# Kernel optimization log

Hardware: AMD Instinct MI355X
Metric: run time of the kernel (lower is better)

The kernel has to match this reference:

```python
import jax, jax.numpy as jnp
import numpy as np

DIM_BODY = 10
DIM_OBJECT = 15
NB_OBJECTS = 3
FIRST_INDS = np.array([0,1,2,3,4,5,6,7,8,9,10,11,12,13,15,16,17,20,21,25])
SECOND_INDS = np.array([0,1,2,3,4,5,6,7,8,9,14,18,19,22,23,24,26,27,28,29])
LOG_SIG_MIN, LOG_SIG_MAX = -20.0, 2.0


def setup_inputs() -> dict:
    key = jax.random.key(0)
    ks = jax.random.split(key, 16)
    B = 65536
    s = 0.05  # weight scale, keeps activations sane
    return {
        "obs": jax.random.normal(ks[0], (B, DIM_BODY + NB_OBJECTS * DIM_OBJECT), jnp.float32),
        "ag": jax.random.normal(ks[1], (B, 30), jnp.float32),
        "g": jax.random.normal(ks[2], (B, 30), jnp.float32),
        "phi_w1": jax.random.normal(ks[3], (80, 256), jnp.float32) * s,
        "phi_b1": jnp.zeros((256,), jnp.float32),
        "phi_w2": jax.random.normal(ks[4], (256, 256), jnp.float32) * s,
        "phi_b2": jnp.zeros((256,), jnp.float32),
        "rho_w1": jax.random.normal(ks[5], (256, 256), jnp.float32) * s,
        "rho_b1": jnp.zeros((256,), jnp.float32),
        "mean_w": jax.random.normal(ks[6], (256, 4), jnp.float32) * s,
        "mean_b": jnp.zeros((4,), jnp.float32),
        "logstd_w": jax.random.normal(ks[7], (256, 4), jnp.float32) * s,
        "logstd_b": jnp.zeros((4,), jnp.float32),
    }


def reference(obs, ag, g, phi_w1, phi_b1, phi_w2, phi_b2, rho_w1, rho_b1,
              mean_w, mean_b, logstd_w, logstd_b):
    body = obs[:, :DIM_BODY]  # [B,10]
    objs = [obs[:, DIM_BODY + DIM_OBJECT * i: DIM_BODY + DIM_OBJECT * (i + 1)]
            for i in range(NB_OBJECTS)]
    ag_f, g_f = ag[:, FIRST_INDS], g[:, FIRST_INDS]
    ag_s, g_s = ag[:, SECOND_INDS], g[:, SECOND_INDS]
    pair_inputs = []
    for i in range(NB_OBJECTS):
        for j in range(NB_OBJECTS):
            if i < j:
                pair_inputs.append(jnp.concatenate([ag_f, body, g_f, objs[i], objs[j]], axis=1))
            elif j < i:
                pair_inputs.append(jnp.concatenate([ag_s, body, g_s, objs[i], objs[j]], axis=1))
    inp = jnp.stack(pair_inputs)  # [6, B, 80]
    # shared phi MLP (2 layers, ReLU on both)
    h = jax.nn.relu(jnp.einsum('pbi,ih->pbh', inp, phi_w1) + phi_b1)
    phi = jax.nn.relu(jnp.einsum('pbh,ho->pbo', h, phi_w2) + phi_b2)
    agg = phi.sum(axis=0)  # [B, 256] sum over pairs
    # rho head
    hr = jax.nn.relu(agg @ rho_w1 + rho_b1)
    mean = hr @ mean_w + mean_b
    logstd = jnp.clip(hr @ logstd_w + logstd_b, LOG_SIG_MIN, LOG_SIG_MAX)
    return mean, logstd
```

## Files before the change

### kernel.cpp

```cpp
#include <hip/hip_runtime.h>
#include <hip/hip_bf16.h>


#define B_TOTAL 65536
#define TROWS   64

typedef __attribute__((ext_vector_type(8)))  short s8v;
typedef __attribute__((ext_vector_type(16))) float f16v;

__constant__ int c_PI[6] = {0,0,1,1,2,2};
__constant__ int c_PJ[6] = {1,2,0,2,0,1};
__constant__ int c_PF[6] = {0,0,1,0,1,1};
__constant__ int c_INV[2][30] = {
  {0,1,2,3,4,5,6,7,8,9,10,11,12,13,-1,14,15,16,-1,-1,17,18,-1,-1,-1,19,-1,-1,-1,-1},
  {0,1,2,3,4,5,6,7,8,9,-1,-1,-1,-1,10,-1,-1,-1,11,12,-1,-1,13,14,15,-1,16,17,18,19}};

static __device__ __forceinline__ short bf16s(float v) {
  __hip_bfloat16 h = __float2bfloat16(v);
  union { __hip_bfloat16 h; short s; } u; u.h = h; return u.s;
}
static __device__ __forceinline__ unsigned pk2(float a, float b) {
  __hip_bfloat162 h = __float22bfloat162_rn(float2{a, b});
  union { __hip_bfloat162 h2; unsigned u; } cv; cv.h2 = h;
  return cv.u;
}

__global__ __launch_bounds__(256)
void prep_weights(const float* __restrict__ phi_w1,
                  const float* __restrict__ phi_b1,
                  const float* __restrict__ phi_w2,
                  const float* __restrict__ rho_w1,
                  const float* __restrict__ mean_w,
                  const float* __restrict__ logstd_w,
                  __hip_bfloat16* __restrict__ W1P,
                  __hip_bfloat16* __restrict__ W2f,
                  __hip_bfloat16* __restrict__ W3f,
                  __hip_bfloat16* __restrict__ W4f) {
  const int wid  = (blockIdx.x * blockDim.x + threadIdx.x) >> 6;
  const int lane = threadIdx.x & 63;
  const int l31  = lane & 31;
  const int kq   = (lane >> 5) * 8;
  if (wid >= 656) return;
  union { short s[8]; s8v v; } o;
  __hip_bfloat16* dst;
  if (wid < 384) {
    const int p = wid >> 6, rem = wid & 63;
    const int n = ((rem >> 3) * 32) + l31;
    const int ksb = (rem & 7) * 16;
    const int f = c_PF[p], oi = c_PI[p], oj = c_PJ[p];
#pragma unroll
    for (int j = 0; j < 8; ++j) {
      int k = ksb + kq + j;
      float v = 0.0f;
      if (k < 30)       { int t = c_INV[f][k];      if (t >= 0) v = phi_w1[t * 256 + n]; }
      else if (k < 60)  { int t = c_INV[f][k - 30]; if (t >= 0) v = phi_w1[(30 + t) * 256 + n]; }
      else if (k < 70)  { v = phi_w1[(20 + k - 60) * 256 + n]; }
      else if (k < 115) { int q = (k - 70) / 15, t = (k - 70) - q * 15;
                          int c = (q == oi) ? 50 + t : (q == oj) ? 65 + t : -1;
                          if (c >= 0) v = phi_w1[c * 256 + n]; }
      else if (k == 115) v = phi_b1[n];
      o.s[j] = bf16s(v);
    }
    dst = W1P + wid * 512 + lane * 8;
  } else if (wid < 512) {
    const int r = wid - 384;
    const int n = ((r >> 4) * 32) + l31;
    const int ksb = (r & 15) * 16;
#pragma unroll
    for (int j = 0; j < 8; ++j)
      o.s[j] = bf16s(phi_w2[(ksb + kq + j) * 256 + n]);
    dst = W2f + r * 512 + lane * 8;
  } else if (wid < 640) {
    const int r = wid - 512;
    const int n = ((r >> 4) * 32) + l31;
    const int ksb = (r & 15) * 16;
#pragma unroll
    for (int j = 0; j < 8; ++j)
      o.s[j] = bf16s(rho_w1[(ksb + kq + j) * 256 + n]);
    dst = W3f + r * 512 + lane * 8;
  } else {
    const int ks = wid - 640;
    const int n = l31;
#pragma unroll
    for (int j = 0; j < 8; ++j) {
      int k = ks * 16 + kq + j;
      float v = (n < 4) ? mean_w[k * 4 + n]
              : (n < 8) ? logstd_w[k * 4 + (n - 4)] : 0.0f;
      o.s[j] = bf16s(v);
    }
    dst = W4f + ks * 512 + lane * 8;
  }
  *reinterpret_cast<s8v*>(dst) = o.v;
}

__global__ __launch_bounds__(512, 1)
void actor_main(const float* __restrict__ obs, const float* __restrict__ ag,
                const float* __restrict__ g,
                const __hip_bfloat16* __restrict__ W1P,
                const __hip_bfloat16* __restrict__ W2f,
                const __hip_bfloat16* __restrict__ W3f,
                const __hip_bfloat16* __restrict__ W4f,
                const float* __restrict__ b2, const float* __restrict__ b3,
                const float* __restrict__ meanb,
                const float* __restrict__ logstdb,
                float* __restrict__ out) {
  __shared__ __align__(16) __hip_bfloat16 rawS[2 * 8 * 512];
  __shared__ __align__(16) __hip_bfloat16 Hs[2][2 * 16 * 512];

  const int tid  = threadIdx.x;
  const int lane = tid & 63;
  const int w    = tid >> 6;
  const int l31  = lane & 31;
  const int q5   = lane >> 5;
  const int r0   = blockIdx.x * TROWS;

  float4 b2v[4];
#pragma unroll
  for (int gidx = 0; gidx < 4; ++gidx)
    b2v[gidx] = *(const float4*)&b2[w * 32 + 8 * gidx + 4 * q5];

  s8v w2f[16];
#pragma unroll
  for (int ks = 0; ks < 16; ++ks)
    w2f[ks] = *(const s8v*)&W2f[(w * 16 + ks) * 512 + lane * 8];

  {
    const int row = tid & 63;
    const int c0  = (tid >> 6) * 16;
    const float* agr = ag  + (size_t)(r0 + row) * 30;
    const float* gr  = g   + (size_t)(r0 + row) * 30;
    const float* obr = obs + (size_t)(r0 + row) * 55;
    union { short s[16]; s8v v[2]; } o;
#pragma unroll
    for (int cc = 0; cc < 16; ++cc) {
      int c = c0 + cc;
      float v;
      if      (c < 30)  v = agr[c];
      else if (c < 60)  v = gr[c - 30];
      else if (c < 115) v = obr[c - 60];
      else if (c == 115) v = 1.0f;
      else              v = 0.0f;
      o.s[cc] = bf16s(v);
    }
    const int base = ((row >> 5) * 8 + (c0 >> 4)) * 512 + (row & 31) * 8;
    *reinterpret_cast<s8v*>(&rawS[base])       = o.v[0];
    *reinterpret_cast<s8v*>(&rawS[base + 256]) = o.v[1];
  }

  f16v agg[2] = {};

  __syncthreads();

  auto gemm1 = [&](int p) {
    const __hip_bfloat16* wb = W1P + p * 32768;
    __hip_bfloat16* buf = &Hs[p & 1][0];
    f16v a1[2] = {};
#pragma unroll
    for (int ks = 0; ks < 8; ++ks) {
      s8v w1 = *(const s8v*)&wb[(w * 8 + ks) * 512 + lane * 8];
      s8v rb0 = *(const s8v*)&rawS[ks * 512 + lane * 8];
      s8v rb1 = *(const s8v*)&rawS[(8 + ks) * 512 + lane * 8];
      a1[0] = __builtin_amdgcn_mfma_f32_32x32x16_bf16(w1, rb0, a1[0], 0, 0, 0);
      a1[1] = __builtin_amdgcn_mfma_f32_32x32x16_bf16(w1, rb1, a1[1], 0, 0, 0);
    }
#pragma unroll
    for (int nt = 0; nt < 2; ++nt)
#pragma unroll
      for (int gp = 0; gp < 4; ++gp) {
        float v0 = fmaxf(a1[nt][4 * gp + 0], 0.f);
        float v1 = fmaxf(a1[nt][4 * gp + 1], 0.f);
        float v2 = fmaxf(a1[nt][4 * gp + 2], 0.f);
        float v3 = fmaxf(a1[nt][4 * gp + 3], 0.f);
        uint2 U; U.x = pk2(v0, v1); U.y = pk2(v2, v3);
        *reinterpret_cast<uint2*>(
          &buf[(nt * 16 + w * 2 + (gp >> 1)) * 512 +
               (l31 + 32 * (gp & 1)) * 8 + 4 * q5]) = U;
      }
  };

  gemm1(0);
  __syncthreads();

#pragma unroll 1
  for (int p = 0; p < 6; ++p) {
    const __hip_bfloat16* buf = &Hs[p & 1][0];
    f16v a2[2] = {};
#pragma unroll
    for (int ks = 0; ks < 16; ++ks) {
      s8v h0 = *(const s8v*)&buf[ks * 512 + lane * 8];
      s8v h1 = *(const s8v*)&buf[(16 + ks) * 512 + lane * 8];
      a2[0] = __builtin_amdgcn_mfma_f32_32x32x16_bf16(w2f[ks], h0, a2[0], 0, 0, 0);
      a2[1] = __builtin_amdgcn_mfma_f32_32x32x16_bf16(w2f[ks], h1, a2[1], 0, 0, 0);
    }
#pragma unroll
    for (int nt = 0; nt < 2; ++nt)
#pragma unroll
      for (int e = 0; e < 16; ++e)
        agg[nt][e] += fmaxf(a2[nt][e] + (&b2v[e >> 2].x)[e & 3], 0.f);

    if (p < 5) gemm1(p + 1);
    __syncthreads();
  }

  s8v w3f[16];
#pragma unroll
  for (int ks = 0; ks < 16; ++ks)
    w3f[ks] = *(const s8v*)&W3f[(w * 16 + ks) * 512 + lane * 8];
  float4 b3v[4];
#pragma unroll
  for (int gidx = 0; gidx < 4; ++gidx)
    b3v[gidx] = *(const float4*)&b3[w * 32 + 8 * gidx + 4 * q5];

  {
    __hip_bfloat16* bufA = &Hs[0][0];
#pragma unroll
    for (int nt = 0; nt < 2; ++nt)
#pragma unroll
      for (int gp = 0; gp < 4; ++gp) {
        uint2 U;
        U.x = pk2(agg[nt][4 * gp + 0], agg[nt][4 * gp + 1]);
        U.y = pk2(agg[nt][4 * gp + 2], agg[nt][4 * gp + 3]);
        *reinterpret_cast<uint2*>(
          &bufA[(nt * 16 + w * 2 + (gp >> 1)) * 512 +
                (l31 + 32 * (gp & 1)) * 8 + 4 * q5]) = U;
      }
  }
  __syncthreads();

  {
    const __hip_bfloat16* bufA = &Hs[0][0];
    f16v a3[2] = {};
#pragma unroll
    for (int ks = 0; ks < 16; ++ks) {
      s8v h0 = *(const s8v*)&bufA[ks * 512 + lane * 8];
      s8v h1 = *(const s8v*)&bufA[(16 + ks) * 512 + lane * 8];
      a3[0] = __builtin_amdgcn_mfma_f32_32x32x16_bf16(w3f[ks], h0, a3[0], 0, 0, 0);
      a3[1] = __builtin_amdgcn_mfma_f32_32x32x16_bf16(w3f[ks], h1, a3[1], 0, 0, 0);
    }
    __hip_bfloat16* bufB = &Hs[1][0];
#pragma unroll
    for (int nt = 0; nt < 2; ++nt)
#pragma unroll
      for (int gp = 0; gp < 4; ++gp) {
        float v0 = fmaxf(a3[nt][4 * gp + 0] + b3v[gp].x, 0.f);
        float v1 = fmaxf(a3[nt][4 * gp + 1] + b3v[gp].y, 0.f);
        float v2 = fmaxf(a3[nt][4 * gp + 2] + b3v[gp].z, 0.f);
        float v3 = fmaxf(a3[nt][4 * gp + 3] + b3v[gp].w, 0.f);
        uint2 U; U.x = pk2(v0, v1); U.y = pk2(v2, v3);
        *reinterpret_cast<uint2*>(
          &bufB[(nt * 16 + w * 2 + (gp >> 1)) * 512 +
                (l31 + 32 * (gp & 1)) * 8 + 4 * q5]) = U;
      }
  }
  __syncthreads();

  if (w < 2) {
    const __hip_bfloat16* bufB = &Hs[1][0];
    f16v a4 = {};
#pragma unroll
    for (int ks = 0; ks < 16; ++ks) {
      s8v w4 = *(const s8v*)&W4f[ks * 512 + lane * 8];
      s8v hf = *(const s8v*)&bufB[(w * 16 + ks) * 512 + lane * 8];
      a4 = __builtin_amdgcn_mfma_f32_32x32x16_bf16(w4, hf, a4, 0, 0, 0);
    }
    const int row = r0 + w * 32 + l31;
    if (q5 == 0) {
      float4 mb = *(const float4*)meanb;
      float4 o;
      o.x = a4[0] + mb.x; o.y = a4[1] + mb.y;
      o.z = a4[2] + mb.z; o.w = a4[3] + mb.w;
      *reinterpret_cast<float4*>(&out[(size_t)row * 4]) = o;
    } else {
      float4 lb = *(const float4*)logstdb;
      float4 o;
      o.x = fminf(fmaxf(a4[0] + lb.x, -20.f), 2.f);
      o.y = fminf(fmaxf(a4[1] + lb.y, -20.f), 2.f);
      o.z = fminf(fmaxf(a4[2] + lb.z, -20.f), 2.f);
      o.w = fminf(fmaxf(a4[3] + lb.w, -20.f), 2.f);
      *reinterpret_cast<float4*>(&out[(size_t)B_TOTAL * 4 + (size_t)row * 4]) = o;
    }
  }
}

extern "C" void kernel_launch(void* const* d_in, const int* in_sizes, int n_in,
                              void* d_out, int out_size, void* d_ws, size_t ws_size,
                              hipStream_t stream) {
  const float* obs      = (const float*)d_in[0];
  const float* ag       = (const float*)d_in[1];
  const float* g        = (const float*)d_in[2];
  const float* phi_w1   = (const float*)d_in[3];
  const float* phi_b1   = (const float*)d_in[4];
  const float* phi_w2   = (const float*)d_in[5];
  const float* phi_b2   = (const float*)d_in[6];
  const float* rho_w1   = (const float*)d_in[7];
  const float* rho_b1   = (const float*)d_in[8];
  const float* mean_w   = (const float*)d_in[9];
  const float* mean_b   = (const float*)d_in[10];
  const float* logstd_w = (const float*)d_in[11];
  const float* logstd_b = (const float*)d_in[12];
  float* out = (float*)d_out;

  char* ws = (char*)d_ws;
  __hip_bfloat16* W1P = (__hip_bfloat16*)(ws);
  __hip_bfloat16* W2f = (__hip_bfloat16*)(ws + 393216);
  __hip_bfloat16* W3f = (__hip_bfloat16*)(ws + 393216 + 131072);
  __hip_bfloat16* W4f = (__hip_bfloat16*)(ws + 393216 + 262144);

  prep_weights<<<164, 256, 0, stream>>>(phi_w1, phi_b1, phi_w2, rho_w1,
                                        mean_w, logstd_w, W1P, W2f, W3f, W4f);
  actor_main<<<B_TOTAL / TROWS, 512, 0, stream>>>(
      obs, ag, g, W1P, W2f, W3f, W4f, phi_b2, rho_b1, mean_b, logstd_b, out);
}
```

Measured before the change: 189.3 us.

## Halve row tile to 32 with 4 waves each owning 64 output columns

Each block now handles 32 rows with 256 threads. Each wave computes two 32-column output tiles against a single row tile, instead of one column tile against two row tiles, and the launch bounds allow two blocks per CU. Register-resident W2 fragments double per wave and are reused for W3 after the pair loop. Biases are now loaded from global memory inside the epilogue. The aim is more blocks in flight and better latency hiding. The cost is that weights are reloaded for twice as many blocks and register pressure per wave rises.

```diff
diff --git a/kernel.cpp b/kernel.cpp
--- a/kernel.cpp
+++ b/kernel.cpp
@@ -3,7 +3,7 @@
 
 
 #define B_TOTAL 65536
-#define TROWS   64
+#define TROWS   32
 
 typedef __attribute__((ext_vector_type(8)))  short s8v;
 typedef __attribute__((ext_vector_type(16))) float f16v;
@@ -93,7 +93,7 @@
   *reinterpret_cast<s8v*>(dst) = o.v;
 }
 
-__global__ __launch_bounds__(512, 1)
+__global__ __launch_bounds__(256, 2)
 void actor_main(const float* __restrict__ obs, const float* __restrict__ ag,
                 const float* __restrict__ g,
                 const __hip_bfloat16* __restrict__ W1P,
@@ -104,8 +104,8 @@
                 const float* __restrict__ meanb,
                 const float* __restrict__ logstdb,
                 float* __restrict__ out) {
-  __shared__ __align__(16) __hip_bfloat16 rawS[2 * 8 * 512];
-  __shared__ __align__(16) __hip_bfloat16 Hs[2][2 * 16 * 512];
+  __shared__ __align__(16) __hip_bfloat16 rawS[8 * 512];
+  __shared__ __align__(16) __hip_bfloat16 Hs[2][16 * 512];
 
   const int tid  = threadIdx.x;
   const int lane = tid & 63;
@@ -114,19 +114,16 @@
   const int q5   = lane >> 5;
   const int r0   = blockIdx.x * TROWS;
 
-  float4 b2v[4];
-#pragma unroll
-  for (int gidx = 0; gidx < 4; ++gidx)
-    b2v[gidx] = *(const float4*)&b2[w * 32 + 8 * gidx + 4 * q5];
-
-  s8v w2f[16];
-#pragma unroll
-  for (int ks = 0; ks < 16; ++ks)
-    w2f[ks] = *(const s8v*)&W2f[(w * 16 + ks) * 512 + lane * 8];
+  s8v w2f[16][2];
+#pragma unroll
+  for (int ct = 0; ct < 2; ++ct)
+#pragma unroll
+    for (int ks = 0; ks < 16; ++ks)
+      w2f[ks][ct] = *(const s8v*)&W2f[((w * 2 + ct) * 16 + ks) * 512 + lane * 8];
 
   {
-    const int row = tid & 63;
-    const int c0  = (tid >> 6) * 16;
+    const int row = tid & 31;
+    const int c0  = (tid >> 5) * 16;
     const float* agr = ag  + (size_t)(r0 + row) * 30;
     const float* gr  = g   + (size_t)(r0 + row) * 30;
     const float* obr = obs + (size_t)(r0 + row) * 55;
@@ -142,7 +139,7 @@
       else              v = 0.0f;
       o.s[cc] = bf16s(v);
     }
-    const int base = ((row >> 5) * 8 + (c0 >> 4)) * 512 + (row & 31) * 8;
+    const int base = (c0 >> 4) * 512 + row * 8;
     *reinterpret_cast<s8v*>(&rawS[base])       = o.v[0];
     *reinterpret_cast<s8v*>(&rawS[base + 256]) = o.v[1];
   }
@@ -157,23 +154,23 @@
     f16v a1[2] = {};
 #pragma unroll
     for (int ks = 0; ks < 8; ++ks) {
-      s8v w1 = *(const s8v*)&wb[(w * 8 + ks) * 512 + lane * 8];
-      s8v rb0 = *(const s8v*)&rawS[ks * 512 + lane * 8];
-      s8v rb1 = *(const s8v*)&rawS[(8 + ks) * 512 + lane * 8];
-      a1[0] = __builtin_amdgcn_mfma_f32_32x32x16_bf16(w1, rb0, a1[0], 0, 0, 0);
-      a1[1] = __builtin_amdgcn_mfma_f32_32x32x16_bf16(w1, rb1, a1[1], 0, 0, 0);
-    }
-#pragma unroll
-    for (int nt = 0; nt < 2; ++nt)
+      s8v rb = *(const s8v*)&rawS[ks * 512 + lane * 8];
+      s8v w10 = *(const s8v*)&wb[((w * 2 + 0) * 8 + ks) * 512 + lane * 8];
+      s8v w11 = *(const s8v*)&wb[((w * 2 + 1) * 8 + ks) * 512 + lane * 8];
+      a1[0] = __builtin_amdgcn_mfma_f32_32x32x16_bf16(w10, rb, a1[0], 0, 0, 0);
+      a1[1] = __builtin_amdgcn_mfma_f32_32x32x16_bf16(w11, rb, a1[1], 0, 0, 0);
+    }
+#pragma unroll
+    for (int ct = 0; ct < 2; ++ct)
 #pragma unroll
       for (int gp = 0; gp < 4; ++gp) {
-        float v0 = fmaxf(a1[nt][4 * gp + 0], 0.f);
-        float v1 = fmaxf(a1[nt][4 * gp + 1], 0.f);
-        float v2 = fmaxf(a1[nt][4 * gp + 2], 0.f);
-        float v3 = fmaxf(a1[nt][4 * gp + 3], 0.f);
+        float v0 = fmaxf(a1[ct][4 * gp + 0], 0.f);
+        float v1 = fmaxf(a1[ct][4 * gp + 1], 0.f);
+        float v2 = fmaxf(a1[ct][4 * gp + 2], 0.f);
+        float v3 = fmaxf(a1[ct][4 * gp + 3], 0.f);
         uint2 U; U.x = pk2(v0, v1); U.y = pk2(v2, v3);
         *reinterpret_cast<uint2*>(
-          &buf[(nt * 16 + w * 2 + (gp >> 1)) * 512 +
+          &buf[(w * 4 + ct * 2 + (gp >> 1)) * 512 +
                (l31 + 32 * (gp & 1)) * 8 + 4 * q5]) = U;
       }
   };
@@ -187,41 +184,42 @@
     f16v a2[2] = {};
 #pragma unroll
     for (int ks = 0; ks < 16; ++ks) {
-      s8v h0 = *(const s8v*)&buf[ks * 512 + lane * 8];
-      s8v h1 = *(const s8v*)&buf[(16 + ks) * 512 + lane * 8];
-      a2[0] = __builtin_amdgcn_mfma_f32_32x32x16_bf16(w2f[ks], h0, a2[0], 0, 0, 0);
-      a2[1] = __builtin_amdgcn_mfma_f32_32x32x16_bf16(w2f[ks], h1, a2[1], 0, 0, 0);
-    }
-#pragma unroll
-    for (int nt = 0; nt < 2; ++nt)
-#pragma unroll
-      for (int e = 0; e < 16; ++e)
-        agg[nt][e] += fmaxf(a2[nt][e] + (&b2v[e >> 2].x)[e & 3], 0.f);
+      s8v hb = *(const s8v*)&buf[ks * 512 + lane * 8];
+      a2[0] = __builtin_amdgcn_mfma_f32_32x32x16_bf16(w2f[ks][0], hb, a2[0], 0, 0, 0);
+      a2[1] = __builtin_amdgcn_mfma_f32_32x32x16_bf16(w2f[ks][1], hb, a2[1], 0, 0, 0);
+    }
+#pragma unroll
+    for (int ct = 0; ct < 2; ++ct)
+#pragma unroll
+      for (int gp = 0; gp < 4; ++gp) {
+        const float4 bb = *(const float4*)&b2[w * 64 + ct * 32 + 8 * gp + 4 * q5];
+        agg[ct][4 * gp + 0] += fmaxf(a2[ct][4 * gp + 0] + bb.x, 0.f);
+        agg[ct][4 * gp + 1] += fmaxf(a2[ct][4 * gp + 1] + bb.y, 0.f);
+        agg[ct][4 * gp + 2] += fmaxf(a2[ct][4 * gp + 2] + bb.z, 0.f);
+        agg[ct][4 * gp + 3] += fmaxf(a2[ct][4 * gp + 3] + bb.w, 0.f);
+      }
 
     if (p < 5) gemm1(p + 1);
     __syncthreads();
   }
 
-  s8v w3f[16];
-#pragma unroll
-  for (int ks = 0; ks < 16; ++ks)
-    w3f[ks] = *(const s8v*)&W3f[(w * 16 + ks) * 512 + lane * 8];
-  float4 b3v[4];
-#pragma unroll
-  for (int gidx = 0; gidx < 4; ++gidx)
-    b3v[gidx] = *(const float4*)&b3[w * 32 + 8 * gidx + 4 * q5];
+#pragma unroll
+  for (int ct = 0; ct < 2; ++ct)
+#pragma unroll
+    for (int ks = 0; ks < 16; ++ks)
+      w2f[ks][ct] = *(const s8v*)&W3f[((w * 2 + ct) * 16 + ks) * 512 + lane * 8];
 
   {
     __hip_bfloat16* bufA = &Hs[0][0];
 #pragma unroll
-    for (int nt = 0; nt < 2; ++nt)
+    for (int ct = 0; ct < 2; ++ct)
 #pragma unroll
       for (int gp = 0; gp < 4; ++gp) {
         uint2 U;
-        U.x = pk2(agg[nt][4 * gp + 0], agg[nt][4 * gp + 1]);
-        U.y = pk2(agg[nt][4 * gp + 2], agg[nt][4 * gp + 3]);
+        U.x = pk2(agg[ct][4 * gp + 0], agg[ct][4 * gp + 1]);
+        U.y = pk2(agg[ct][4 * gp + 2], agg[ct][4 * gp + 3]);
         *reinterpret_cast<uint2*>(
-          &bufA[(nt * 16 + w * 2 + (gp >> 1)) * 512 +
+          &bufA[(w * 4 + ct * 2 + (gp >> 1)) * 512 +
                 (l31 + 32 * (gp & 1)) * 8 + 4 * q5]) = U;
       }
   }
@@ -232,38 +230,38 @@
     f16v a3[2] = {};
 #pragma unroll
     for (int ks = 0; ks < 16; ++ks) {
-      s8v h0 = *(const s8v*)&bufA[ks * 512 + lane * 8];
-      s8v h1 = *(const s8v*)&bufA[(16 + ks) * 512 + lane * 8];
-      a3[0] = __builtin_amdgcn_mfma_f32_32x32x16_bf16(w3f[ks], h0, a3[0], 0, 0, 0);
-      a3[1] = __builtin_amdgcn_mfma_f32_32x32x16_bf16(w3f[ks], h1, a3[1], 0, 0, 0);
+      s8v hb = *(const s8v*)&bufA[ks * 512 + lane * 8];
+      a3[0] = __builtin_amdgcn_mfma_f32_32x32x16_bf16(w2f[ks][0], hb, a3[0], 0, 0, 0);
+      a3[1] = __builtin_amdgcn_mfma_f32_32x32x16_bf16(w2f[ks][1], hb, a3[1], 0, 0, 0);
     }
     __hip_bfloat16* bufB = &Hs[1][0];
 #pragma unroll
-    for (int nt = 0; nt < 2; ++nt)
+    for (int ct = 0; ct < 2; ++ct)
 #pragma unroll
       for (int gp = 0; gp < 4; ++gp) {
-        float v0 = fmaxf(a3[nt][4 * gp + 0] + b3v[gp].x, 0.f);
-        float v1 = fmaxf(a3[nt][4 * gp + 1] + b3v[gp].y, 0.f);
-        float v2 = fmaxf(a3[nt][4 * gp + 2] + b3v[gp].z, 0.f);
-        float v3 = fmaxf(a3[nt][4 * gp + 3] + b3v[gp].w, 0.f);
+        const float4 bb = *(const float4*)&b3[w * 64 + ct * 32 + 8 * gp + 4 * q5];
+        float v0 = fmaxf(a3[ct][4 * gp + 0] + bb.x, 0.f);
+        float v1 = fmaxf(a3[ct][4 * gp + 1] + bb.y, 0.f);
+        float v2 = fmaxf(a3[ct][4 * gp + 2] + bb.z, 0.f);
+        float v3 = fmaxf(a3[ct][4 * gp + 3] + bb.w, 0.f);
         uint2 U; U.x = pk2(v0, v1); U.y = pk2(v2, v3);
         *reinterpret_cast<uint2*>(
-          &bufB[(nt * 16 + w * 2 + (gp >> 1)) * 512 +
+          &bufB[(w * 4 + ct * 2 + (gp >> 1)) * 512 +
                 (l31 + 32 * (gp & 1)) * 8 + 4 * q5]) = U;
       }
   }
   __syncthreads();
 
-  if (w < 2) {
+  if (w == 0) {
     const __hip_bfloat16* bufB = &Hs[1][0];
     f16v a4 = {};
 #pragma unroll
     for (int ks = 0; ks < 16; ++ks) {
       s8v w4 = *(const s8v*)&W4f[ks * 512 + lane * 8];
-      s8v hf = *(const s8v*)&bufB[(w * 16 + ks) * 512 + lane * 8];
+      s8v hf = *(const s8v*)&bufB[ks * 512 + lane * 8];
       a4 = __builtin_amdgcn_mfma_f32_32x32x16_bf16(w4, hf, a4, 0, 0, 0);
     }
-    const int row = r0 + w * 32 + l31;
+    const int row = r0 + l31;
     if (q5 == 0) {
       float4 mb = *(const float4*)meanb;
       float4 o;
@@ -308,6 +306,6 @@
 
   prep_weights<<<164, 256, 0, stream>>>(phi_w1, phi_b1, phi_w2, rho_w1,
                                         mean_w, logstd_w, W1P, W2f, W3f, W4f);
-  actor_main<<<B_TOTAL / TROWS, 512, 0, stream>>>(
+  actor_main<<<B_TOTAL / TROWS, 256, 0, stream>>>(
       obs, ag, g, W1P, W2f, W3f, W4f, phi_b2, rho_b1, mean_b, logstd_b, out);
 }
```

New measurement: 297.6 us. 1.57x slower.
